# Kernel tuning notes

Hardware: AMD Instinct MI355X
Metric: run time of the kernel (lower is better)

Reference implementation:

```python
import jax, jax.numpy as jnp
import numpy as np

N = 100000   # nodes
E = 1600000  # edges
F = 128      # input features
D = 128      # hidden dim
L = 3        # layers
G = 128      # graphs in batch
C = 2        # classes
BN_EPS = 1e-5


def setup_inputs() -> dict:
    key = jax.random.key(0)
    ks = jax.random.split(key, 20)
    s = 1.0 / np.sqrt(D)
    inp = {
        "x": jax.random.normal(ks[0], (N, F), jnp.float32),
        "edge_index": jax.random.randint(ks[1], (2, E), 0, N),
        "node_weight": jax.random.uniform(ks[2], (N,), jnp.float32),
        "batch": jnp.sort(jax.random.randint(ks[3], (N,), 0, G)),
        # GIN MLP params, stacked over layers (all square since F == D)
        "W1": jax.random.normal(ks[4], (L, F, D), jnp.float32) * s,
        "b1": jnp.zeros((L, D), jnp.float32),
        "g1": jnp.ones((L, D), jnp.float32),
        "bt1": jnp.zeros((L, D), jnp.float32),
        "W2": jax.random.normal(ks[5], (L, D, D), jnp.float32) * s,
        "b2": jnp.zeros((L, D), jnp.float32),
        "g2": jnp.ones((L, D), jnp.float32),
        "bt2": jnp.zeros((L, D), jnp.float32),
        # outer per-layer BatchNorm
        "og": jnp.ones((L, D), jnp.float32),
        "ob": jnp.zeros((L, D), jnp.float32),
        # final classifier
        "fcW": jax.random.normal(ks[6], (D, C), jnp.float32) * s,
        "fcb": jnp.zeros((C,), jnp.float32),
    }
    return inp


def _bn(h, gamma, beta):
    # training-mode BatchNorm1d over nodes: biased variance, eps=1e-5
    m = jnp.mean(h, axis=0)
    v = jnp.var(h, axis=0)
    return (h - m) * jax.lax.rsqrt(v + BN_EPS) * gamma + beta


def reference(x, edge_index, node_weight, batch,
              W1, b1, g1, bt1, W2, b2, g2, bt2, og, ob, fcW, fcb):
    src, dst = edge_index[0], edge_index[1]  # messages flow src -> dst (PyG)
    for l in range(L):
        # GIN: sum_{j in N(i)} x_j + (1 + eps) * x_i,  eps = 0 (non-trainable)
        agg = jax.ops.segment_sum(x[src], dst, num_segments=N)
        h = agg + x
        # nn = Linear -> BN -> Linear -> BN
        h = _bn(h @ W1[l] + b1[l], g1[l], bt1[l])
        h = _bn(h @ W2[l] + b2[l], g2[l], bt2[l])
        # outer BN + ReLU (dropout p=0 is identity)
        x = jax.nn.relu(_bn(h, og[l], ob[l]))
    node_embeddings = x
    graph_embedding = jax.ops.segment_sum(
        node_embeddings * node_weight[:, None], batch, num_segments=G)
    out = graph_embedding @ fcW + fcb
    return (node_embeddings, graph_embedding, out)
```

## Files before the change

### kernel.cpp

```cpp
#include <hip/hip_runtime.h>

#define N_NODES 100000
#define N_EDGES 1600000
#define DF 128
#define NL 3
#define NG 128
#define NC 2
#define BN_EPS 1e-5f
#define GEMM_BLOCKS ((N_NODES + 127) / 128)
#define GE_SLICES 16

#define NBKT 98
#define NBIN_BLOCKS 512
#define EDGES_PER_BLOCK (N_EDGES / NBIN_BLOCKS)

typedef unsigned int u32;
typedef unsigned short u16;
typedef unsigned long long u64;

using bf16x8 = __attribute__((ext_vector_type(8))) short;
using f32x4  = __attribute__((ext_vector_type(4))) float;

__device__ __forceinline__ u16 f2bf(float f) {
    u32 u = __float_as_uint(f);
    u32 r = (u + 0x7FFFu + ((u >> 16) & 1u)) >> 16;
    return (u16)r;
}
__device__ __forceinline__ float bflo(u32 v) { return __uint_as_float(v << 16); }
__device__ __forceinline__ float bfhi(u32 v) { return __uint_as_float(v & 0xFFFF0000u); }

__global__ __launch_bounds__(256) void cvt_x_kernel(const float* __restrict__ x,
                                                    u16* __restrict__ xb) {
    size_t i4 = (size_t)blockIdx.x * 256 + threadIdx.x;
    float4 v = ((const float4*)x)[i4];
    u32 lo = (u32)f2bf(v.x) | ((u32)f2bf(v.y) << 16);
    u32 hi = (u32)f2bf(v.z) | ((u32)f2bf(v.w) << 16);
    ((uint2*)xb)[i4] = make_uint2(lo, hi);
}

__global__ __launch_bounds__(256) void bin_count_kernel(const int* __restrict__ dst,
                                                        int* __restrict__ blkhist) {
    __shared__ int hist[NBKT];
    int t = threadIdx.x, b = blockIdx.x;
    for (int i = t; i < NBKT; i += 256) hist[i] = 0;
    __syncthreads();
    int base = b * EDGES_PER_BLOCK;
    for (int i = t; i < EDGES_PER_BLOCK; i += 256)
        atomicAdd(&hist[dst[base + i] >> 10], 1);
    __syncthreads();
    for (int i = t; i < NBKT; i += 256) blkhist[i * NBIN_BLOCKS + b] = hist[i];
}

__global__ __launch_bounds__(512) void binscanA_kernel(int* __restrict__ blkhist,
                                                       int* __restrict__ bkt_total) {
    __shared__ int buf[NBIN_BLOCKS];
    int bucket = blockIdx.x, t = threadIdx.x;
    int v = blkhist[bucket * NBIN_BLOCKS + t];
    buf[t] = v;
    __syncthreads();
    for (int off = 1; off < NBIN_BLOCKS; off <<= 1) {
        int tv = (t >= off) ? buf[t - off] : 0;
        __syncthreads();
        buf[t] += tv;
        __syncthreads();
    }
    blkhist[bucket * NBIN_BLOCKS + t] = buf[t] - v;
    if (t == NBIN_BLOCKS - 1) bkt_total[bucket] = buf[t];
}

__global__ __launch_bounds__(128) void binscanB_kernel(const int* __restrict__ bkt_total,
                                                       int* __restrict__ bktbase) {
    __shared__ int buf[128];
    int t = threadIdx.x;
    int v = (t < NBKT) ? bkt_total[t] : 0;
    buf[t] = v;
    __syncthreads();
    for (int off = 1; off < 128; off <<= 1) {
        int tv = (t >= off) ? buf[t - off] : 0;
        __syncthreads();
        buf[t] += tv;
        __syncthreads();
    }
    if (t < NBKT) bktbase[t] = buf[t] - v;
    if (t == NBKT - 1) bktbase[NBKT] = buf[t];
}

__global__ __launch_bounds__(256) void bin_scatter_kernel(const int* __restrict__ src,
                                                          const int* __restrict__ dst,
                                                          const int* __restrict__ blkhist,
                                                          const int* __restrict__ bktbase,
                                                          u64* __restrict__ pairs) {
    __shared__ int lofs[NBKT];
    int t = threadIdx.x, b = blockIdx.x;
    for (int i = t; i < NBKT; i += 256)
        lofs[i] = bktbase[i] + blkhist[i * NBIN_BLOCKS + b];
    __syncthreads();
    int base = b * EDGES_PER_BLOCK;
    for (int i = t; i < EDGES_PER_BLOCK; i += 256) {
        int d = dst[base + i];
        int s = src[base + i];
        int p = atomicAdd(&lofs[d >> 10], 1);
        pairs[p] = ((u64)(u32)d << 32) | (u32)s;
    }
}

__global__ __launch_bounds__(1024) void csr_build_kernel(const u64* __restrict__ pairs,
                                                         const int* __restrict__ bktbase,
                                                         int* __restrict__ offsets,
                                                         int* __restrict__ adj) {
    __shared__ int cnt[1024];
    __shared__ int buf[1024];
    int b = blockIdx.x, t = threadIdx.x;
    int nbase = b << 10;
    int pb = bktbase[b], pe = bktbase[b + 1];
    cnt[t] = 0;
    __syncthreads();
    for (int i = pb + t; i < pe; i += 1024)
        atomicAdd(&cnt[(int)(pairs[i] >> 32) - nbase], 1);
    __syncthreads();
    int v = cnt[t];
    buf[t] = v;
    __syncthreads();
    for (int off = 1; off < 1024; off <<= 1) {
        int tv = (t >= off) ? buf[t - off] : 0;
        __syncthreads();
        buf[t] += tv;
        __syncthreads();
    }
    int excl = buf[t] - v;
    int node = nbase + t;
    if (node < N_NODES) offsets[node] = pb + excl;
    if (b == NBKT - 1 && t == 0) offsets[N_NODES] = N_EDGES;
    cnt[t] = excl;
    __syncthreads();
    for (int i = pb + t; i < pe; i += 1024) {
        u64 pr = pairs[i];
        int d = (int)(pr >> 32);
        int pos = atomicAdd(&cnt[d - nbase], 1);
        adj[pb + pos] = (int)(pr & 0xFFFFFFFFu);
    }
}

__global__ __launch_bounds__(256) void agg_kernel(const u32* __restrict__ X,
                                                  const int* __restrict__ offsets,
                                                  const int* __restrict__ adj,
                                                  u32* __restrict__ out) {
    int node = blockIdx.x * 4 + (threadIdx.x >> 6);
    int l = threadIdx.x & 63;
    const u32* Xl = X + l;
    u32 v = Xl[(size_t)node << 6];
    float s0 = bflo(v), s1 = bfhi(v);
    float t0 = 0.f, t1 = 0.f;
    int k = offsets[node], e = offsets[node + 1];
    for (; k + 8 <= e; k += 8) {
        int a0 = adj[k + 0], a1 = adj[k + 1], a2 = adj[k + 2], a3 = adj[k + 3];
        int a4 = adj[k + 4], a5 = adj[k + 5], a6 = adj[k + 6], a7 = adj[k + 7];
        u32 u0 = Xl[(size_t)a0 << 6];
        u32 u1 = Xl[(size_t)a1 << 6];
        u32 u2 = Xl[(size_t)a2 << 6];
        u32 u3 = Xl[(size_t)a3 << 6];
        u32 u4 = Xl[(size_t)a4 << 6];
        u32 u5 = Xl[(size_t)a5 << 6];
        u32 u6 = Xl[(size_t)a6 << 6];
        u32 u7 = Xl[(size_t)a7 << 6];
        s0 += bflo(u0); s1 += bfhi(u0);
        t0 += bflo(u1); t1 += bfhi(u1);
        s0 += bflo(u2); s1 += bfhi(u2);
        t0 += bflo(u3); t1 += bfhi(u3);
        s0 += bflo(u4); s1 += bfhi(u4);
        t0 += bflo(u5); t1 += bfhi(u5);
        s0 += bflo(u6); s1 += bfhi(u6);
        t0 += bflo(u7); t1 += bfhi(u7);
    }
    if (k + 4 <= e) {
        int a0 = adj[k + 0], a1 = adj[k + 1], a2 = adj[k + 2], a3 = adj[k + 3];
        u32 u0 = Xl[(size_t)a0 << 6];
        u32 u1 = Xl[(size_t)a1 << 6];
        u32 u2 = Xl[(size_t)a2 << 6];
        u32 u3 = Xl[(size_t)a3 << 6];
        s0 += bflo(u0); s1 += bfhi(u0);
        t0 += bflo(u1); t1 += bfhi(u1);
        s0 += bflo(u2); s1 += bfhi(u2);
        t0 += bflo(u3); t1 += bfhi(u3);
        k += 4;
    }
    for (; k < e; k++) {
        u32 u = Xl[(size_t)adj[k] << 6];
        s0 += bflo(u); s1 += bfhi(u);
    }
    out[((size_t)node << 6) + l] = (u32)f2bf(s0 + t0) | ((u32)f2bf(s1 + t1) << 16);
}

template <int OUT_BF16>
__global__ __launch_bounds__(256) void gemm_mfma_kernel(const u16* __restrict__ A,
                                                        const u16* __restrict__ Wt,
                                                        const float* __restrict__ bias,
                                                        void* __restrict__ outp,
                                                        float* __restrict__ psumB,
                                                        float* __restrict__ psqB, int nrows) {
    __shared__ __align__(16) u16 sW[16384];

    int tid = threadIdx.x;
    int rb = blockIdx.x * 128;

    {
        const uint4* g = (const uint4*)Wt;
#pragma unroll
        for (int p = 0; p < 8; p++) {
            int q = p * 256 + tid;
            int r = q >> 4, seg = q & 15;
            uint4 v = g[q];
            *(uint4*)((char*)sW + r * 256 + ((seg * 16) ^ ((r & 7) << 4))) = v;
        }
    }

    int l = tid & 63, w = tid >> 6;
    int lr = l & 15, lg = l >> 4;

    bf16x8 afr[2][4];
#pragma unroll
    for (int t = 0; t < 2; t++) {
        int grow = rb + w * 32 + t * 16 + lr;
        bool ok = grow < nrows;
#pragma unroll
        for (int kc = 0; kc < 4; kc++) {
            bf16x8 z = {0, 0, 0, 0, 0, 0, 0, 0};
            if (ok) z = *(const bf16x8*)(A + (size_t)grow * 128 + kc * 32 + lg * 8);
            afr[t][kc] = z;
        }
    }
    __syncthreads();

    f32x4 acc[2][8];
#pragma unroll
    for (int t = 0; t < 2; t++)
#pragma unroll
        for (int c = 0; c < 8; c++) acc[t][c] = (f32x4){0.f, 0.f, 0.f, 0.f};

#pragma unroll
    for (int kc = 0; kc < 4; kc++) {
        int kb2 = (kc * 32 + lg * 8) * 2;
        bf16x8 b[8];
#pragma unroll
        for (int c = 0; c < 8; c++) {
            int col = c * 16 + lr;
            b[c] = *(const bf16x8*)((const char*)sW + col * 256 + (kb2 ^ ((col & 7) << 4)));
        }
#pragma unroll
        for (int t = 0; t < 2; t++)
#pragma unroll
            for (int c = 0; c < 8; c++)
                acc[t][c] = __builtin_amdgcn_mfma_f32_16x16x32_bf16(afr[t][kc], b[c], acc[t][c], 0, 0, 0);
    }

    float bb[8];
#pragma unroll
    for (int c = 0; c < 8; c++) bb[c] = bias[c * 16 + lr];

    float sp[8], qp[8];
#pragma unroll
    for (int c = 0; c < 8; c++) { sp[c] = 0.f; qp[c] = 0.f; }

    float* outF = (float*)outp;
    u16* outB = (u16*)outp;
#pragma unroll
    for (int t = 0; t < 2; t++) {
#pragma unroll
        for (int r = 0; r < 4; r++) {
            int grow = rb + w * 32 + t * 16 + lg * 4 + r;
            bool ok = grow < nrows;
#pragma unroll
            for (int c = 0; c < 8; c++) {
                float v = acc[t][c][r] + bb[c];
                if (ok) {
                    int col = c * 16 + lr;
                    if (OUT_BF16)
                        outB[(size_t)grow * 128 + col] = f2bf(v);
                    else
                        outF[(size_t)grow * 128 + col] = v;
                    sp[c] += v;
                    qp[c] += v * v;
                }
            }
        }
    }
#pragma unroll
    for (int c = 0; c < 8; c++) {
        sp[c] += __shfl_xor(sp[c], 16); sp[c] += __shfl_xor(sp[c], 32);
        qp[c] += __shfl_xor(qp[c], 16); qp[c] += __shfl_xor(qp[c], 32);
    }
    __syncthreads();
    float* sred = (float*)sW;
    if (lg == 0) {
#pragma unroll
        for (int c = 0; c < 8; c++) {
            sred[(((w * 8 + c) * 16) + lr) * 2 + 0] = sp[c];
            sred[(((w * 8 + c) * 16) + lr) * 2 + 1] = qp[c];
        }
    }
    __syncthreads();
    if (tid < 128) {
        int c = tid >> 4, r = tid & 15;
        float s = 0.f, q = 0.f;
#pragma unroll
        for (int ww = 0; ww < 4; ww++) {
            s += sred[(((ww * 8 + c) * 16) + r) * 2 + 0];
            q += sred[(((ww * 8 + c) * 16) + r) * 2 + 1];
        }
        psumB[blockIdx.x * 128 + tid] = s;
        psqB[blockIdx.x * 128 + tid] = q;
    }
}

__global__ __launch_bounds__(256) void stats_reduce_kernel(const float* __restrict__ psumB,
                                                           const float* __restrict__ psqB,
                                                           float* __restrict__ outS,
                                                           float* __restrict__ outQ) {
    int f = blockIdx.x;
    int t = threadIdx.x;
    float s = 0.f, q = 0.f;
    for (int b = t; b < GEMM_BLOCKS; b += 256) {
        s += psumB[b * 128 + f];
        q += psqB[b * 128 + f];
    }
#pragma unroll
    for (int off = 1; off < 64; off <<= 1) {
        s += __shfl_xor(s, off);
        q += __shfl_xor(q, off);
    }
    __shared__ float rs[4], rq[4];
    int w = t >> 6;
    if ((t & 63) == 0) { rs[w] = s; rq[w] = q; }
    __syncthreads();
    if (t == 0) {
        outS[f] = rs[0] + rs[1] + rs[2] + rs[3];
        outQ[f] = rq[0] + rq[1] + rq[2] + rq[3];
    }
}

__global__ __launch_bounds__(128) void bnfold_kernel(const float* __restrict__ psum,
                                                     const float* __restrict__ psq,
                                                     const float* __restrict__ g,
                                                     const float* __restrict__ bt,
                                                     const float* __restrict__ W2,
                                                     const float* __restrict__ b2,
                                                     u16* __restrict__ W2ft,
                                                     float* __restrict__ b2f) {
    __shared__ float sc1[128], sh1[128];
    int k = threadIdx.x;
    int j = blockIdx.x;
    {
        float S = psum[k], Q = psq[k];
        float m = S / (float)N_NODES;
        float v = Q / (float)N_NODES - m * m;
        if (v < 0.f) v = 0.f;
        float r = rsqrtf(v + BN_EPS);
        float sc = r * g[k];
        sc1[k] = sc;
        sh1[k] = bt[k] - m * sc;
    }
    __syncthreads();
    float w = W2[k * 128 + j];
    W2ft[j * 128 + k] = f2bf(sc1[k] * w);
    float p = sh1[k] * w;
#pragma unroll
    for (int off = 1; off < 64; off <<= 1) p += __shfl_xor(p, off);
    __shared__ float r2[2];
    if ((k & 63) == 0) r2[k >> 6] = p;
    __syncthreads();
    if (k == 0) b2f[j] = b2[j] + r2[0] + r2[1];
}

__global__ __launch_bounds__(128) void bnfin2_kernel(const float* __restrict__ psum,
                                                     const float* __restrict__ psq,
                                                     const float* __restrict__ g,
                                                     const float* __restrict__ bt,
                                                     const float* __restrict__ og,
                                                     const float* __restrict__ ob,
                                                     float* __restrict__ scale,
                                                     float* __restrict__ shift) {
    int f = threadIdx.x;
    float S = psum[f], Q = psq[f];
    float m = S / (float)N_NODES;
    float v = Q / (float)N_NODES - m * m;
    if (v < 0.f) v = 0.f;
    float r2 = rsqrtf(v + BN_EPS);
    float a = r2 * g[f];
    float vu = v * a * a;
    float r3 = rsqrtf(vu + BN_EPS);
    float sc = a * r3 * og[f];
    scale[f] = sc;
    shift[f] = ob[f] - m * sc;
}

__global__ void w1_prep_kernel(const float* __restrict__ W, u16* __restrict__ Wt) {
    int q = blockIdx.x * 256 + threadIdx.x;
    int layer = q >> 14;
    int r = q & 16383;
    int j = r >> 7, k = r & 127;
    Wt[q] = f2bf(W[layer * 16384 + k * 128 + j]);
}

__global__ __launch_bounds__(256) void relu_affine_bf16_kernel(const u16* __restrict__ Hb,
                                                               const float* __restrict__ scale,
                                                               const float* __restrict__ shift,
                                                               u16* __restrict__ xb) {
    size_t i4 = (size_t)blockIdx.x * 256 + threadIdx.x;
    int fb = ((int)(i4 & 31)) * 4;
    uint2 hv = ((const uint2*)Hb)[i4];
    float4 sc = *(const float4*)&scale[fb];
    float4 sh = *(const float4*)&shift[fb];
    float y0 = fmaxf(bflo(hv.x) * sc.x + sh.x, 0.f);
    float y1 = fmaxf(bfhi(hv.x) * sc.y + sh.y, 0.f);
    float y2 = fmaxf(bflo(hv.y) * sc.z + sh.z, 0.f);
    float y3 = fmaxf(bfhi(hv.y) * sc.w + sh.w, 0.f);
    u32 lo = (u32)f2bf(y0) | ((u32)f2bf(y1) << 16);
    u32 hi = (u32)f2bf(y2) | ((u32)f2bf(y3) << 16);
    ((uint2*)xb)[i4] = make_uint2(lo, hi);
}

__global__ __launch_bounds__(256) void relu_affine_final_kernel(float* __restrict__ H,
                                                                const float* __restrict__ scale,
                                                                const float* __restrict__ shift) {
    size_t i4 = (size_t)blockIdx.x * 256 + threadIdx.x;
    int fb = ((int)(i4 & 31)) * 4;
    float4 h = ((const float4*)H)[i4];
    float4 sc = *(const float4*)&scale[fb];
    float4 sh = *(const float4*)&shift[fb];
    float4 y;
    y.x = fmaxf(h.x * sc.x + sh.x, 0.f);
    y.y = fmaxf(h.y * sc.y + sh.y, 0.f);
    y.z = fmaxf(h.z * sc.z + sh.z, 0.f);
    y.w = fmaxf(h.w * sc.w + sh.w, 0.f);
    ((float4*)H)[i4] = y;
}

__global__ __launch_bounds__(128) void graph_embed_part_kernel(const float* __restrict__ X,
                                                               const float* __restrict__ w,
                                                               const int* __restrict__ batch,
                                                               float* __restrict__ gpart) {
    int g = blockIdx.x;
    int sl = blockIdx.y;
    int f = threadIdx.x;
    int lo = 0, hi = N_NODES;
    while (lo < hi) { int mid = (lo + hi) >> 1; if (batch[mid] < g) lo = mid + 1; else hi = mid; }
    int s = lo;
    lo = 0; hi = N_NODES;
    while (lo < hi) { int mid = (lo + hi) >> 1; if (batch[mid] < g + 1) lo = mid + 1; else hi = mid; }
    int e = lo;
    int cnt = e - s;
    int per = (cnt + GE_SLICES - 1) / GE_SLICES;
    int rs = s + sl * per;
    int re = rs + per; if (re > e) re = e;
    float acc = 0.f;
    for (int r = rs; r < re; r++) acc += X[(size_t)r * DF + f] * w[r];
    gpart[((size_t)g * GE_SLICES + sl) * DF + f] = acc;
}

__global__ __launch_bounds__(128) void graph_embed_reduce_kernel(const float* __restrict__ gpart,
                                                                 float* __restrict__ ge) {
    int g = blockIdx.x, f = threadIdx.x;
    float a = 0.f;
#pragma unroll
    for (int s = 0; s < GE_SLICES; s++) a += gpart[((size_t)g * GE_SLICES + s) * DF + f];
    ge[g * DF + f] = a;
}

__global__ void final_fc_kernel(const float* __restrict__ ge, const float* __restrict__ fcW,
                                const float* __restrict__ fcb, float* __restrict__ out) {
    int idx = blockIdx.x * blockDim.x + threadIdx.x;
    if (idx < NG * NC) {
        int g = idx / NC, c = idx % NC;
        float acc = fcb[c];
        for (int d = 0; d < DF; d++) acc += ge[g * DF + d] * fcW[d * NC + c];
        out[idx] = acc;
    }
}

extern "C" void kernel_launch(void* const* d_in, const int* in_sizes, int n_in,
                              void* d_out, int out_size, void* d_ws, size_t ws_size,
                              hipStream_t stream) {
    const float* x    = (const float*)d_in[0];
    const int*   ei   = (const int*)d_in[1];
    const int*   src  = ei;
    const int*   dst  = ei + N_EDGES;
    const float* nw   = (const float*)d_in[2];
    const int*   batch= (const int*)d_in[3];
    const float* W1   = (const float*)d_in[4];
    const float* b1   = (const float*)d_in[5];
    const float* g1   = (const float*)d_in[6];
    const float* bt1  = (const float*)d_in[7];
    const float* W2   = (const float*)d_in[8];
    const float* b2   = (const float*)d_in[9];
    const float* g2   = (const float*)d_in[10];
    const float* bt2  = (const float*)d_in[11];
    const float* og   = (const float*)d_in[12];
    const float* ob   = (const float*)d_in[13];
    const float* fcW  = (const float*)d_in[14];
    const float* fcb  = (const float*)d_in[15];

    float* out_f    = (float*)d_out;
    float* node_out = out_f;
    float* ge       = out_f + (size_t)N_NODES * DF;
    float* cls      = ge + NG * DF;

    char* w = (char*)d_ws;
    auto alloc = [&](size_t bytes) { char* p = w; w += (bytes + 255) & ~(size_t)255; return p; };

    u16*   XB      = (u16*)alloc((size_t)N_NODES * DF * 2);
    u16*   AGG     = (u16*)alloc((size_t)N_NODES * DF * 2);
    u16*   H1      = (u16*)alloc((size_t)N_NODES * DF * 2);
    int*   offsets = (int*)alloc((size_t)(N_NODES + 1) * 4);
    int*   adj     = (int*)alloc((size_t)N_EDGES * 4);
    float* psumB   = (float*)alloc((size_t)GEMM_BLOCKS * 128 * 4);
    float* psqB    = (float*)alloc((size_t)GEMM_BLOCKS * 128 * 4);
    float* sF      = (float*)alloc(128 * 4);
    float* qF      = (float*)alloc(128 * 4);
    u16*   W1t     = (u16*)alloc((size_t)NL * 16384 * 2);
    u16*   W2ft    = (u16*)alloc(16384 * 2);
    float* b2f     = (float*)alloc(128 * 4);
    float* scaleO  = (float*)alloc(128 * 4);
    float* shiftO  = (float*)alloc(128 * 4);
    float* gpart   = (float*)alloc((size_t)NG * GE_SLICES * DF * 4);
    int*   blkhist = (int*)alloc((size_t)NBKT * NBIN_BLOCKS * 4);
    int*   bkt_tot = (int*)alloc(NBKT * 4);
    int*   bktbase = (int*)alloc((NBKT + 1) * 4);

    u64* pairs = (u64*)AGG;

    cvt_x_kernel<<<12500, 256, 0, stream>>>(x, XB);
    w1_prep_kernel<<<192, 256, 0, stream>>>(W1, W1t);

    bin_count_kernel<<<NBIN_BLOCKS, 256, 0, stream>>>(dst, blkhist);
    binscanA_kernel<<<NBKT, NBIN_BLOCKS, 0, stream>>>(blkhist, bkt_tot);
    binscanB_kernel<<<1, 128, 0, stream>>>(bkt_tot, bktbase);
    bin_scatter_kernel<<<NBIN_BLOCKS, 256, 0, stream>>>(src, dst, blkhist, bktbase, pairs);
    csr_build_kernel<<<NBKT, 1024, 0, stream>>>(pairs, bktbase, offsets, adj);

    for (int l = 0; l < NL; l++) {
        agg_kernel<<<N_NODES / 4, 256, 0, stream>>>((const u32*)XB, offsets, adj, (u32*)AGG);
        gemm_mfma_kernel<1><<<GEMM_BLOCKS, 256, 0, stream>>>(AGG, W1t + (size_t)l * 16384,
                                                             b1 + l * DF, H1, psumB, psqB,
                                                             N_NODES);
        stats_reduce_kernel<<<128, 256, 0, stream>>>(psumB, psqB, sF, qF);
        bnfold_kernel<<<128, 128, 0, stream>>>(sF, qF, g1 + l * DF, bt1 + l * DF,
                                               W2 + (size_t)l * DF * DF, b2 + l * DF, W2ft, b2f);
        if (l < NL - 1) {
            gemm_mfma_kernel<1><<<GEMM_BLOCKS, 256, 0, stream>>>(H1, W2ft, b2f, AGG,
                                                                 psumB, psqB, N_NODES);
        } else {
            gemm_mfma_kernel<0><<<GEMM_BLOCKS, 256, 0, stream>>>(H1, W2ft, b2f, node_out,
                                                                 psumB, psqB, N_NODES);
        }
        stats_reduce_kernel<<<128, 256, 0, stream>>>(psumB, psqB, sF, qF);
        bnfin2_kernel<<<1, 128, 0, stream>>>(sF, qF, g2 + l * DF, bt2 + l * DF,
                                             og + l * DF, ob + l * DF, scaleO, shiftO);
        if (l < NL - 1) {
            relu_affine_bf16_kernel<<<12500, 256, 0, stream>>>(AGG, scaleO, shiftO, XB);
        } else {
            relu_affine_final_kernel<<<12500, 256, 0, stream>>>(node_out, scaleO, shiftO);
        }
    }

    graph_embed_part_kernel<<<dim3(NG, GE_SLICES), 128, 0, stream>>>(node_out, nw, batch, gpart);
    graph_embed_reduce_kernel<<<NG, 128, 0, stream>>>(gpart, ge);
    final_fc_kernel<<<1, 256, 0, stream>>>(ge, fcW, fcb, cls);
}
```

Measured before the change: 467.8 us.

## Store node features in feature-plane chunks for cache-friendly gather aggregation

Node features are now written in 8 feature planes of 16 bf16 values (32 bytes per node), and the aggregation kernel assigns each block one plane, so 8 nodes are handled per wave with 8 lanes each. Each plane's working set is smaller and more likely to stay in cache during the random neighbour gathers, and the GEMM reads its A operand from the chunked layout. The aggregation loop becomes a wave-uniform predicated loop with four accumulators, which costs divergence when neighbour counts differ within a wave. The second BN finalisation is also folded into the stats reduction kernel, removing one launch.

```diff
diff --git a/kernel.cpp b/kernel.cpp
--- a/kernel.cpp
+++ b/kernel.cpp
@@ -30,12 +30,16 @@
 __device__ __forceinline__ float bfhi(u32 v) { return __uint_as_float(v & 0xFFFF0000u); }
 
 __global__ __launch_bounds__(256) void cvt_x_kernel(const float* __restrict__ x,
-                                                    u16* __restrict__ xb) {
+                                                    u16* __restrict__ Xc) {
     size_t i4 = (size_t)blockIdx.x * 256 + threadIdx.x;
+    int seg = (int)(i4 & 31);
+    size_t node = i4 >> 5;
     float4 v = ((const float4*)x)[i4];
     u32 lo = (u32)f2bf(v.x) | ((u32)f2bf(v.y) << 16);
     u32 hi = (u32)f2bf(v.z) | ((u32)f2bf(v.w) << 16);
-    ((uint2*)xb)[i4] = make_uint2(lo, hi);
+    int p = seg >> 2;
+    *(uint2*)((char*)Xc + (size_t)p * (N_NODES * 32) + node * 32 + (seg & 3) * 8) =
+        make_uint2(lo, hi);
 }
 
 __global__ __launch_bounds__(256) void bin_count_kernel(const int* __restrict__ dst,
@@ -141,57 +145,44 @@
     }
 }
 
-__global__ __launch_bounds__(256) void agg_kernel(const u32* __restrict__ X,
+__global__ __launch_bounds__(256) void agg_kernel(const u32* __restrict__ Xc,
                                                   const int* __restrict__ offsets,
                                                   const int* __restrict__ adj,
-                                                  u32* __restrict__ out) {
-    int node = blockIdx.x * 4 + (threadIdx.x >> 6);
-    int l = threadIdx.x & 63;
-    const u32* Xl = X + l;
-    u32 v = Xl[(size_t)node << 6];
+                                                  u32* __restrict__ outc) {
+    int plane = blockIdx.x & 7;
+    int grp = blockIdx.x >> 3;
+    int t = threadIdx.x;
+    int wid = t >> 6, lane = t & 63;
+    int fpos = lane & 7, nslot = lane >> 3;
+    int node = (grp * 4 + wid) * 8 + nslot;
+    const u32* Xp = Xc + (size_t)plane * (N_NODES * 8) + fpos;
+    u32* Op = outc + (size_t)plane * (N_NODES * 8) + fpos;
+    u32 v = Xp[(size_t)node * 8];
     float s0 = bflo(v), s1 = bfhi(v);
-    float t0 = 0.f, t1 = 0.f;
+    float t0 = 0.f, t1 = 0.f, u0s = 0.f, u1s = 0.f, w0 = 0.f, w1 = 0.f;
     int k = offsets[node], e = offsets[node + 1];
-    for (; k + 8 <= e; k += 8) {
-        int a0 = adj[k + 0], a1 = adj[k + 1], a2 = adj[k + 2], a3 = adj[k + 3];
-        int a4 = adj[k + 4], a5 = adj[k + 5], a6 = adj[k + 6], a7 = adj[k + 7];
-        u32 u0 = Xl[(size_t)a0 << 6];
-        u32 u1 = Xl[(size_t)a1 << 6];
-        u32 u2 = Xl[(size_t)a2 << 6];
-        u32 u3 = Xl[(size_t)a3 << 6];
-        u32 u4 = Xl[(size_t)a4 << 6];
-        u32 u5 = Xl[(size_t)a5 << 6];
-        u32 u6 = Xl[(size_t)a6 << 6];
-        u32 u7 = Xl[(size_t)a7 << 6];
-        s0 += bflo(u0); s1 += bfhi(u0);
-        t0 += bflo(u1); t1 += bfhi(u1);
-        s0 += bflo(u2); s1 += bfhi(u2);
-        t0 += bflo(u3); t1 += bfhi(u3);
-        s0 += bflo(u4); s1 += bfhi(u4);
-        t0 += bflo(u5); t1 += bfhi(u5);
-        s0 += bflo(u6); s1 += bfhi(u6);
-        t0 += bflo(u7); t1 += bfhi(u7);
-    }
-    if (k + 4 <= e) {
-        int a0 = adj[k + 0], a1 = adj[k + 1], a2 = adj[k + 2], a3 = adj[k + 3];
-        u32 u0 = Xl[(size_t)a0 << 6];
-        u32 u1 = Xl[(size_t)a1 << 6];
-        u32 u2 = Xl[(size_t)a2 << 6];
-        u32 u3 = Xl[(size_t)a3 << 6];
-        s0 += bflo(u0); s1 += bfhi(u0);
-        t0 += bflo(u1); t1 += bfhi(u1);
-        s0 += bflo(u2); s1 += bfhi(u2);
-        t0 += bflo(u3); t1 += bfhi(u3);
+    int a0 = (k + 0 < e) ? adj[k + 0] : -1;
+    int a1 = (k + 1 < e) ? adj[k + 1] : -1;
+    int a2 = (k + 2 < e) ? adj[k + 2] : -1;
+    int a3 = (k + 3 < e) ? adj[k + 3] : -1;
+    while (__any(a0 >= 0)) {
+        int b0 = (k + 4 < e) ? adj[k + 4] : -1;
+        int b1 = (k + 5 < e) ? adj[k + 5] : -1;
+        int b2 = (k + 6 < e) ? adj[k + 6] : -1;
+        int b3 = (k + 7 < e) ? adj[k + 7] : -1;
+        if (a0 >= 0) { u32 u = Xp[(size_t)a0 * 8]; s0 += bflo(u); s1 += bfhi(u); }
+        if (a1 >= 0) { u32 u = Xp[(size_t)a1 * 8]; t0 += bflo(u); t1 += bfhi(u); }
+        if (a2 >= 0) { u32 u = Xp[(size_t)a2 * 8]; u0s += bflo(u); u1s += bfhi(u); }
+        if (a3 >= 0) { u32 u = Xp[(size_t)a3 * 8]; w0 += bflo(u); w1 += bfhi(u); }
+        a0 = b0; a1 = b1; a2 = b2; a3 = b3;
         k += 4;
     }
-    for (; k < e; k++) {
-        u32 u = Xl[(size_t)adj[k] << 6];
-        s0 += bflo(u); s1 += bfhi(u);
-    }
-    out[((size_t)node << 6) + l] = (u32)f2bf(s0 + t0) | ((u32)f2bf(s1 + t1) << 16);
-}
-
-template <int OUT_BF16>
+    s0 += t0 + u0s + w0;
+    s1 += t1 + u1s + w1;
+    Op[(size_t)node * 8] = (u32)f2bf(s0) | ((u32)f2bf(s1) << 16);
+}
+
+template <int OUT_BF16, int A_CHUNKED>
 __global__ __launch_bounds__(256) void gemm_mfma_kernel(const u16* __restrict__ A,
                                                         const u16* __restrict__ Wt,
                                                         const float* __restrict__ bias,
@@ -225,7 +216,15 @@
 #pragma unroll
         for (int kc = 0; kc < 4; kc++) {
             bf16x8 z = {0, 0, 0, 0, 0, 0, 0, 0};
-            if (ok) z = *(const bf16x8*)(A + (size_t)grow * 128 + kc * 32 + lg * 8);
+            if (ok) {
+                if (A_CHUNKED) {
+                    int plane = 2 * kc + (lg >> 1);
+                    z = *(const bf16x8*)(A + (size_t)plane * (N_NODES * 16) +
+                                         (size_t)grow * 16 + (lg & 1) * 8);
+                } else {
+                    z = *(const bf16x8*)(A + (size_t)grow * 128 + kc * 32 + lg * 8);
+                }
+            }
             afr[t][kc] = z;
         }
     }
@@ -312,8 +311,13 @@
     }
 }
 
+template <int MODE>
 __global__ __launch_bounds__(256) void stats_reduce_kernel(const float* __restrict__ psumB,
                                                            const float* __restrict__ psqB,
+                                                           const float* __restrict__ g,
+                                                           const float* __restrict__ bt,
+                                                           const float* __restrict__ og,
+                                                           const float* __restrict__ ob,
                                                            float* __restrict__ outS,
                                                            float* __restrict__ outQ) {
     int f = blockIdx.x;
@@ -333,8 +337,23 @@
     if ((t & 63) == 0) { rs[w] = s; rq[w] = q; }
     __syncthreads();
     if (t == 0) {
-        outS[f] = rs[0] + rs[1] + rs[2] + rs[3];
-        outQ[f] = rq[0] + rq[1] + rq[2] + rq[3];
+        float S = rs[0] + rs[1] + rs[2] + rs[3];
+        float Q = rq[0] + rq[1] + rq[2] + rq[3];
+        if (MODE == 0) {
+            outS[f] = S;
+            outQ[f] = Q;
+        } else {
+            float m = S / (float)N_NODES;
+            float v = Q / (float)N_NODES - m * m;
+            if (v < 0.f) v = 0.f;
+            float r2 = rsqrtf(v + BN_EPS);
+            float a = r2 * g[f];
+            float vu = v * a * a;
+            float r3 = rsqrtf(vu + BN_EPS);
+            float sc = a * r3 * og[f];
+            outS[f] = sc;
+            outQ[f] = ob[f] - m * sc;
+        }
     }
 }
 
@@ -371,28 +390,6 @@
     if (k == 0) b2f[j] = b2[j] + r2[0] + r2[1];
 }
 
-__global__ __launch_bounds__(128) void bnfin2_kernel(const float* __restrict__ psum,
-                                                     const float* __restrict__ psq,
-                                                     const float* __restrict__ g,
-                                                     const float* __restrict__ bt,
-                                                     const float* __restrict__ og,
-                                                     const float* __restrict__ ob,
-                                                     float* __restrict__ scale,
-                                                     float* __restrict__ shift) {
-    int f = threadIdx.x;
-    float S = psum[f], Q = psq[f];
-    float m = S / (float)N_NODES;
-    float v = Q / (float)N_NODES - m * m;
-    if (v < 0.f) v = 0.f;
-    float r2 = rsqrtf(v + BN_EPS);
-    float a = r2 * g[f];
-    float vu = v * a * a;
-    float r3 = rsqrtf(vu + BN_EPS);
-    float sc = a * r3 * og[f];
-    scale[f] = sc;
-    shift[f] = ob[f] - m * sc;
-}
-
 __global__ void w1_prep_kernel(const float* __restrict__ W, u16* __restrict__ Wt) {
     int q = blockIdx.x * 256 + threadIdx.x;
     int layer = q >> 14;
@@ -404,9 +401,11 @@
 __global__ __launch_bounds__(256) void relu_affine_bf16_kernel(const u16* __restrict__ Hb,
                                                                const float* __restrict__ scale,
                                                                const float* __restrict__ shift,
-                                                               u16* __restrict__ xb) {
+                                                               u16* __restrict__ Xc) {
     size_t i4 = (size_t)blockIdx.x * 256 + threadIdx.x;
-    int fb = ((int)(i4 & 31)) * 4;
+    int seg = (int)(i4 & 31);
+    size_t node = i4 >> 5;
+    int fb = seg * 4;
     uint2 hv = ((const uint2*)Hb)[i4];
     float4 sc = *(const float4*)&scale[fb];
     float4 sh = *(const float4*)&shift[fb];
@@ -416,7 +415,9 @@
     float y3 = fmaxf(bfhi(hv.y) * sc.w + sh.w, 0.f);
     u32 lo = (u32)f2bf(y0) | ((u32)f2bf(y1) << 16);
     u32 hi = (u32)f2bf(y2) | ((u32)f2bf(y3) << 16);
-    ((uint2*)xb)[i4] = make_uint2(lo, hi);
+    int p = seg >> 2;
+    *(uint2*)((char*)Xc + (size_t)p * (N_NODES * 32) + node * 32 + (seg & 3) * 8) =
+        make_uint2(lo, hi);
 }
 
 __global__ __launch_bounds__(256) void relu_affine_final_kernel(float* __restrict__ H,
@@ -538,23 +539,24 @@
     csr_build_kernel<<<NBKT, 1024, 0, stream>>>(pairs, bktbase, offsets, adj);
 
     for (int l = 0; l < NL; l++) {
-        agg_kernel<<<N_NODES / 4, 256, 0, stream>>>((const u32*)XB, offsets, adj, (u32*)AGG);
-        gemm_mfma_kernel<1><<<GEMM_BLOCKS, 256, 0, stream>>>(AGG, W1t + (size_t)l * 16384,
-                                                             b1 + l * DF, H1, psumB, psqB,
-                                                             N_NODES);
-        stats_reduce_kernel<<<128, 256, 0, stream>>>(psumB, psqB, sF, qF);
+        agg_kernel<<<(N_NODES / 32) * 8, 256, 0, stream>>>((const u32*)XB, offsets, adj,
+                                                           (u32*)AGG);
+        gemm_mfma_kernel<1, 1><<<GEMM_BLOCKS, 256, 0, stream>>>(AGG, W1t + (size_t)l * 16384,
+                                                                b1 + l * DF, H1, psumB, psqB,
+                                                                N_NODES);
+        stats_reduce_kernel<0><<<128, 256, 0, stream>>>(psumB, psqB, nullptr, nullptr,
+                                                        nullptr, nullptr, sF, qF);
         bnfold_kernel<<<128, 128, 0, stream>>>(sF, qF, g1 + l * DF, bt1 + l * DF,
                                                W2 + (size_t)l * DF * DF, b2 + l * DF, W2ft, b2f);
         if (l < NL - 1) {
-            gemm_mfma_kernel<1><<<GEMM_BLOCKS, 256, 0, stream>>>(H1, W2ft, b2f, AGG,
-                                                                 psumB, psqB, N_NODES);
+            gemm_mfma_kernel<1, 0><<<GEMM_BLOCKS, 256, 0, stream>>>(H1, W2ft, b2f, AGG,
+                                                                    psumB, psqB, N_NODES);
         } else {
-            gemm_mfma_kernel<0><<<GEMM_BLOCKS, 256, 0, stream>>>(H1, W2ft, b2f, node_out,
-                                                                 psumB, psqB, N_NODES);
-        }
-        stats_reduce_kernel<<<128, 256, 0, stream>>>(psumB, psqB, sF, qF);
-        bnfin2_kernel<<<1, 128, 0, stream>>>(sF, qF, g2 + l * DF, bt2 + l * DF,
-                                             og + l * DF, ob + l * DF, scaleO, shiftO);
+            gemm_mfma_kernel<0, 0><<<GEMM_BLOCKS, 256, 0, stream>>>(H1, W2ft, b2f, node_out,
+                                                                    psumB, psqB, N_NODES);
+        }
+        stats_reduce_kernel<1><<<128, 256, 0, stream>>>(psumB, psqB, g2 + l * DF, bt2 + l * DF,
+                                                        og + l * DF, ob + l * DF, scaleO, shiftO);
         if (l < NL - 1) {
             relu_affine_bf16_kernel<<<12500, 256, 0, stream>>>(AGG, scaleO, shiftO, XB);
         } else {
```

After: 581.5 us. 1.24x slower.
